# Kernel optimization log

Measured on AMD Instinct MI355X. Metric: run time of the kernel, lower is better.

## Reference

```python
import jax, jax.numpy as jnp
import numpy as np

N = 50000      # nodes
E = 800000     # directed edges (before self loops)
IN = 128       # in_channels
H = 4          # heads
C = 64         # hidden_channels per head
G = 64         # graphs in batch
SLOPE = 0.2    # PyG GATConv default negative_slope


def setup_inputs() -> dict:
    key = jax.random.key(0)
    ks = jax.random.split(key, 16)
    x = jax.random.normal(ks[0], (N, IN), jnp.float32)
    edge_index = jax.random.randint(ks[1], (2, E), 0, N, dtype=jnp.int32)
    batch = jnp.sort(jax.random.randint(ks[2], (N,), 0, G, dtype=jnp.int32))
    s_in = 1.0 / np.sqrt(IN)
    s_hid = 1.0 / np.sqrt(H * C)
    return {
        "x": x,
        "edge_index": edge_index,
        "batch": batch,
        # layer 1: GATConv(IN -> C, heads=H, concat)
        "W1": jax.random.normal(ks[3], (IN, H * C), jnp.float32) * s_in,
        "a_src1": jax.random.normal(ks[4], (H, C), jnp.float32) * s_hid,
        "a_dst1": jax.random.normal(ks[5], (H, C), jnp.float32) * s_hid,
        "b1": jnp.zeros((H * C,), jnp.float32),
        # layer 2: GATConv(H*C -> C, heads=H, concat)
        "W2": jax.random.normal(ks[6], (H * C, H * C), jnp.float32) * s_hid,
        "a_src2": jax.random.normal(ks[7], (H, C), jnp.float32) * s_hid,
        "a_dst2": jax.random.normal(ks[8], (H, C), jnp.float32) * s_hid,
        "b2": jnp.zeros((H * C,), jnp.float32),
        # classifier head
        "W_lin": jax.random.normal(ks[9], (H * C, 2), jnp.float32) * s_hid,
        "b_lin": jnp.zeros((2,), jnp.float32),
    }


def _gat_conv(x, src, dst, W, a_src, a_dst, b):
    """PyG-style GATConv (concat heads, self-loops already in src/dst)."""
    n = x.shape[0]
    h = (x @ W).reshape(n, H, C)                       # [n, H, C]
    alpha_s = jnp.einsum('nhc,hc->nh', h, a_src)       # [n, H]
    alpha_d = jnp.einsum('nhc,hc->nh', h, a_dst)
    e = alpha_s[src] + alpha_d[dst]                    # [Etot, H]
    e = jnp.where(e > 0, e, SLOPE * e)                 # LeakyReLU
    # segment softmax over edges incoming to each destination node
    e_max = jax.lax.stop_gradient(jax.ops.segment_max(e, dst, num_segments=n))
    ex = jnp.exp(e - e_max[dst])
    denom = jax.ops.segment_sum(ex, dst, num_segments=n)
    alpha = ex / denom[dst]                            # [Etot, H]
    msg = alpha[:, :, None] * h[src]                   # [Etot, H, C]
    out = jax.ops.segment_sum(msg, dst, num_segments=n)
    return out.reshape(n, H * C) + b


def reference(x, edge_index, batch, W1, a_src1, a_dst1, b1,
              W2, a_src2, a_dst2, b2, W_lin, b_lin):
    n = x.shape[0]
    # add self loops (PyG GATConv default add_self_loops=True)
    loop = jnp.arange(n, dtype=edge_index.dtype)
    src = jnp.concatenate([edge_index[0], loop])
    dst = jnp.concatenate([edge_index[1], loop])

    h = _gat_conv(x, src, dst, W1, a_src1, a_dst1, b1)
    h = jax.nn.elu(h)                                  # dropout inactive (eval)
    h = _gat_conv(h, src, dst, W2, a_src2, a_dst2, b2)
    h = jax.nn.elu(h)

    # global mean pool over node-to-graph assignment
    sums = jax.ops.segment_sum(h, batch, num_segments=G)
    cnt = jax.ops.segment_sum(jnp.ones((n,), h.dtype), batch, num_segments=G)
    pooled = sums / jnp.maximum(cnt, 1.0)[:, None]     # [G, H*C]

    return pooled @ W_lin + b_lin                      # [G, 2] logits
```

## Files before the change

### kernel.cpp

```cpp
#include <hip/hip_runtime.h>
#include <hip/hip_bf16.h>
#include <math.h>

#define NN 50000
#define EE 800000
#define IN_CH 128
#define HH 4
#define CC 64
#define GG 64
#define HC 256
#define SLOPE 0.2f

#define NBUK 98
#define BDST 512
#define CAPB 10240
#define CAPD 64

typedef short bf16x8 __attribute__((ext_vector_type(8)));
typedef float f32x4  __attribute__((ext_vector_type(4)));
typedef float f32x2  __attribute__((ext_vector_type(2)));

__device__ inline ushort f2bf(float f) {
    union { __hip_bfloat16 h; ushort u; } c;
    c.h = __float2bfloat16(f);
    return c.u;
}
__device__ inline float bfu(ushort u) {
    union { uint u; float f; } c; c.u = ((uint)u) << 16; return c.f;
}
__device__ inline uchar f2e4m3(float v) {
    return (uchar)(__builtin_amdgcn_cvt_pk_fp8_f32(v, v, 0, false) & 0xff);
}
__device__ inline void pkfma(f32x2& a, f32x2 b, f32x2 c) {
    asm("v_pk_fma_f32 %0, %1, %2, %0" : "+v"(a) : "v"(b), "v"(c));
}


__device__ void conv_body(const float* __restrict__ B, ushort* __restrict__ Bt,
                          int kt, int n0, float (*tile)[33]) {
    int tx = threadIdx.x & 31, ty = threadIdx.x >> 5;
    #pragma unroll
    for (int r = ty; r < 32; r += 8)
        tile[r][tx] = B[(size_t)(kt * 32 + r) * 256 + n0 + tx];
    __syncthreads();
    #pragma unroll
    for (int r = ty; r < 32; r += 8)
        Bt[((size_t)kt * 256 + n0 + r) * 32 + tx] = f2bf(tile[tx][r]);
}

__global__ __launch_bounds__(256) void prep_kernel(const float* __restrict__ W1,
                                                   ushort* __restrict__ Bt1,
                                                   const float* __restrict__ W2,
                                                   ushort* __restrict__ Bt2,
                                                   int* __restrict__ bcnt,
                                                   float* __restrict__ pool,
                                                   float* __restrict__ pcnt) {
    __shared__ float tile[32][33];
    int b = blockIdx.x;
    if (b < 32) {
        conv_body(W1, Bt1, b >> 3, (b & 7) * 32, tile);
    } else if (b < 96) {
        int bb = b - 32;
        conv_body(W2, Bt2, bb >> 3, (bb & 7) * 32, tile);
    } else if (b == 96) {
        int i = threadIdx.x;
        if (i < NBUK) bcnt[i] = 0;
        if (i < GG) pcnt[i] = 0.f;
    } else {
        pool[(b - 97) * 256 + threadIdx.x] = 0.f;
    }
}


__global__ __launch_bounds__(256) void partition_kernel(const int* __restrict__ ei,
                                                        int* __restrict__ bcnt,
                                                        int2* __restrict__ part,
                                                        int total) {
    __shared__ int hist[NBUK];
    __shared__ int base[NBUK];
    int t = threadIdx.x;
    int c0 = blockIdx.x * 2048;
    for (int b = t; b < NBUK; b += 256) hist[b] = 0;
    __syncthreads();
    int s[8], d[8], rk[8], bk[8];
    #pragma unroll
    for (int k = 0; k < 8; ++k) {
        int i = c0 + k * 256 + t;
        rk[k] = -1;
        if (i < total) {
            if (i < EE) { s[k] = ei[i]; d[k] = ei[EE + i]; }
            else        { s[k] = d[k] = i - EE; }
            bk[k] = d[k] >> 9;
            rk[k] = atomicAdd(&hist[bk[k]], 1);
        }
    }
    __syncthreads();
    for (int b = t; b < NBUK; b += 256) {
        int h = hist[b];
        base[b] = h ? atomicAdd(&bcnt[b], h) : 0;
    }
    __syncthreads();
    #pragma unroll
    for (int k = 0; k < 8; ++k) {
        if (rk[k] >= 0) {
            int pos = base[bk[k]] + rk[k];
            if (pos < CAPB)
                part[(size_t)bk[k] * CAPB + pos] = make_int2(s[k], d[k]);
        }
    }
}


__global__ __launch_bounds__(1024) void bucket_csr_kernel(const int* __restrict__ bcnt,
                                                          const int2* __restrict__ part,
                                                          ushort* __restrict__ csrb,
                                                          int* __restrict__ cnt_out, int n) {
    __shared__ int cnt[BDST];
    __shared__ ushort rows[BDST * CAPD];
    int b = blockIdx.x, t = threadIdx.x;
    int d0 = b << 9;
    for (int i = t; i < BDST; i += 1024) cnt[i] = 0;
    __syncthreads();
    int m = min(bcnt[b], CAPB);
    const int2* pp = part + (size_t)b * CAPB;
    for (int i = t; i < m; i += 1024) {
        int2 e = pp[i];
        int ld = e.y - d0;
        int r = atomicAdd(&cnt[ld], 1);
        if (r < CAPD) rows[(ld << 6) + r] = (ushort)e.x;
    }
    __syncthreads();
    const uint4* src4 = reinterpret_cast<const uint4*>(rows);
    uint4* dst4 = reinterpret_cast<uint4*>(csrb + ((size_t)d0 << 6));
    #pragma unroll
    for (int i = 0; i < 4; ++i) dst4[i * 1024 + t] = src4[i * 1024 + t];
    for (int i = t; i < BDST; i += 1024) {
        int dd = d0 + i;
        if (dd < n) cnt_out[dd] = min(cnt[i], CAPD);
    }
}


template <int K, bool A_BF16>
__global__ __launch_bounds__(256) void mfma_gemm_fused(const void* __restrict__ Ap,
                                                       const ushort* __restrict__ Bt,
                                                       uchar* __restrict__ H8,
                                                       float* __restrict__ as_,
                                                       float* __restrict__ ad_,
                                                       const float* __restrict__ a_src,
                                                       const float* __restrict__ a_dst,
                                                       int M) {
    __shared__ __align__(16) ushort As[64 * 32];
    __shared__ __align__(16) ushort Bs[256 * 32];
    int tid = threadIdx.x;
    int wave = tid >> 6, lane = tid & 63;
    int bm = blockIdx.x * 64;

    f32x4 acc[4][4] = {{}};

    for (int k0 = 0; k0 < K; k0 += 32) {
        {
            int row = tid >> 2, sl = tid & 3;
            int gr = bm + row;
            uint4 q = {0u, 0u, 0u, 0u};
            if (gr < M) {
                if constexpr (A_BF16) {
                    q = *reinterpret_cast<const uint4*>((const ushort*)Ap + (size_t)gr * K + k0 + sl * 8);
                } else {
                    const float* ap = (const float*)Ap + (size_t)gr * K + k0 + sl * 8;
                    float4 f0 = *reinterpret_cast<const float4*>(ap);
                    float4 f1 = *reinterpret_cast<const float4*>(ap + 4);
                    q.x = (uint)f2bf(f0.x) | ((uint)f2bf(f0.y) << 16);
                    q.y = (uint)f2bf(f0.z) | ((uint)f2bf(f0.w) << 16);
                    q.z = (uint)f2bf(f1.x) | ((uint)f2bf(f1.y) << 16);
                    q.w = (uint)f2bf(f1.z) | ((uint)f2bf(f1.w) << 16);
                }
            }
            int ssl = sl ^ ((row >> 1) & 3);
            *reinterpret_cast<uint4*>(&As[row * 32 + ssl * 8]) = q;
        }
        {
            const ushort* bt = Bt + (size_t)(k0 >> 5) * (256 * 32);
            #pragma unroll
            for (int cI = 0; cI < 4; ++cI) {
                int idx = cI * 256 + tid;
                uint4 v = *reinterpret_cast<const uint4*>(bt + idx * 8);
                int n = idx >> 2, sl = idx & 3;
                int ssl = sl ^ ((n >> 1) & 3);
                *reinterpret_cast<uint4*>(&Bs[n * 32 + ssl * 8]) = v;
            }
        }
        __syncthreads();

        int r16 = lane & 15, kg = lane >> 4;
        bf16x8 af[4], bfr[4];
        #pragma unroll
        for (int mi = 0; mi < 4; ++mi) {
            int row = mi * 16 + r16;
            int ssl = kg ^ ((row >> 1) & 3);
            af[mi] = *reinterpret_cast<const bf16x8*>(&As[row * 32 + ssl * 8]);
        }
        #pragma unroll
        for (int ni = 0; ni < 4; ++ni) {
            int n = wave * 64 + ni * 16 + r16;
            int ssl = kg ^ ((n >> 1) & 3);
            bfr[ni] = *reinterpret_cast<const bf16x8*>(&Bs[n * 32 + ssl * 8]);
        }
        #pragma unroll
        for (int mi = 0; mi < 4; ++mi)
            #pragma unroll
            for (int ni = 0; ni < 4; ++ni)
                acc[mi][ni] = __builtin_amdgcn_mfma_f32_16x16x32_bf16(af[mi], bfr[ni], acc[mi][ni], 0, 0, 0);
        __syncthreads();
    }

    int r16 = lane & 15, rg = lane >> 4;
    float asv[4], adv[4];
    #pragma unroll
    for (int ni = 0; ni < 4; ++ni) {
        asv[ni] = a_src[wave * 64 + ni * 16 + r16];
        adv[ni] = a_dst[wave * 64 + ni * 16 + r16];
    }
    #pragma unroll
    for (int mi = 0; mi < 4; ++mi) {
        #pragma unroll
        for (int r = 0; r < 4; ++r) {
            int row = bm + mi * 16 + rg * 4 + r;
            float ps = 0.f, pd = 0.f;
            if (row < M) {
                #pragma unroll
                for (int ni = 0; ni < 4; ++ni) {
                    float v = acc[mi][ni][r];
                    H8[(size_t)row * HC + wave * 64 + ni * 16 + r16] = f2e4m3(v);
                    ps += v * asv[ni];
                    pd += v * adv[ni];
                }
            }
            #pragma unroll
            for (int o = 1; o < 16; o <<= 1) {
                ps += __shfl_xor(ps, o, 64);
                pd += __shfl_xor(pd, o, 64);
            }
            if (row < M && r16 == 0) {
                as_[row * HH + wave] = ps;
                ad_[row * HH + wave] = pd;
            }
        }
    }
}


template <bool OUT_BF16>
__global__ __launch_bounds__(256) void aggregate14_kernel(const uchar* __restrict__ h8,
                                                          const float* __restrict__ as_,
                                                          const float* __restrict__ ad_,
                                                          const int* __restrict__ cnt,
                                                          const ushort* __restrict__ csrb,
                                                          const float* __restrict__ bias,
                                                          void* __restrict__ outp, int n) {
    int w = threadIdx.x >> 6, lane = threadIdx.x & 63;
    int dst = blockIdx.x * 4 + w;
    if (dst >= n) return;
    int es = lane >> 2, hh = lane & 3;
    int ep = lane >> 5, cl = lane & 31;
    int hsel = cl >> 3;

    __shared__ int2 s_pk[4][64][4];

    int deg = cnt[dst];
    int degp = (deg + 7) & ~7;
    const ushort* srcs = csrb + ((size_t)dst << 6);
    float ad = ad_[dst * HH + hh];

    f32x2 accp[4] = {};
    const char* hb = (const char*)h8 + cl * 8;

    int ntile = (degp + 15) >> 4;

    {
        float ew[4]; int sw[4];
        float lm = -INFINITY;
        #pragma unroll
        for (int t = 0; t < 4; ++t) {
            int j = t * 16 + es;
            float e = -INFINITY; int s = 0;
            if (t < ntile && j < deg) {
                s = (int)srcs[j];
                float tv = as_[s * HH + hh] + ad;
                e = fmaxf(tv, tv * SLOPE);
            }
            ew[t] = e; sw[t] = s;
            lm = fmaxf(lm, e);
        }
        #pragma unroll
        for (int o = 4; o < 64; o <<= 1) lm = fmaxf(lm, __shfl_xor(lm, o, 64));
        float den = 0.f;
        #pragma unroll
        for (int t = 0; t < 4; ++t) {
            float wgt = __expf(ew[t] - lm);
            ew[t] = wgt; den += wgt;
        }
        #pragma unroll
        for (int o = 4; o < 64; o <<= 1) den += __shfl_xor(den, o, 64);
        float invden = 1.f / den;
        #pragma unroll
        for (int t = 0; t < 4; ++t) {
            int j = t * 16 + es;
            if (t < ntile && j < degp) {
                s_pk[w][j][hh] = make_int2(__float_as_int(ew[t] * invden), sw[t] << 8);
            }
        }
    }

#define LOADPK(off_, vv, al)                                             \
    {                                                                    \
        int2 pk_ = s_pk[w][jj + (off_) + ep][hsel];                      \
        al = __int_as_float(pk_.x);                                      \
        vv = *reinterpret_cast<const uint2*>(hb + pk_.y);                \
    }

#define DECODE_PK(vv, al)                                                \
    {                                                                    \
        f32x2 ap_; ap_[0] = al; ap_[1] = al;                             \
        f32x2 f_;                                                        \
        f_ = __builtin_amdgcn_cvt_pk_f32_fp8((int)(vv).x, false);        \
        pkfma(accp[0], f_, ap_);                                         \
        f_ = __builtin_amdgcn_cvt_pk_f32_fp8((int)(vv).x, true);         \
        pkfma(accp[1], f_, ap_);                                         \
        f_ = __builtin_amdgcn_cvt_pk_f32_fp8((int)(vv).y, false);        \
        pkfma(accp[2], f_, ap_);                                         \
        f_ = __builtin_amdgcn_cvt_pk_f32_fp8((int)(vv).y, true);         \
        pkfma(accp[3], f_, ap_);                                         \
    }

    for (int jj = 0; jj < degp; jj += 8) {
        uint2 v0, v1, v2, v3;
        float a0, a1, a2, a3;
        LOADPK(0, v0, a0)
        LOADPK(2, v1, a1)
        LOADPK(4, v2, a2)
        LOADPK(6, v3, a3)
        DECODE_PK(v0, a0)
        DECODE_PK(v1, a1)
        DECODE_PK(v2, a2)
        DECODE_PK(v3, a3)
    }
#undef LOADPK
#undef DECODE_PK

    float lo[4] = {accp[0][0], accp[0][1], accp[1][0], accp[1][1]};
    float hi[4] = {accp[2][0], accp[2][1], accp[3][0], accp[3][1]};
    float fin[4];
    #pragma unroll
    for (int k = 0; k < 4; ++k) {
        float send = ep ? lo[k] : hi[k];
        float recv = __shfl_xor(send, 32, 64);
        fin[k] = (ep ? hi[k] : lo[k]) + recv;
    }

    int ch = cl * 8 + ep * 4;
    const float4 b4 = *reinterpret_cast<const float4*>(bias + ch);
    float r0 = fin[0] + b4.x, r1 = fin[1] + b4.y, r2 = fin[2] + b4.z, r3 = fin[3] + b4.w;
    r0 = r0 > 0.f ? r0 : __expf(r0) - 1.f;
    r1 = r1 > 0.f ? r1 : __expf(r1) - 1.f;
    r2 = r2 > 0.f ? r2 : __expf(r2) - 1.f;
    r3 = r3 > 0.f ? r3 : __expf(r3) - 1.f;
    if constexpr (OUT_BF16) {
        uint2 q;
        q.x = (uint)f2bf(r0) | ((uint)f2bf(r1) << 16);
        q.y = (uint)f2bf(r2) | ((uint)f2bf(r3) << 16);
        *reinterpret_cast<uint2*>((ushort*)outp + (size_t)dst * HC + ch) = q;
    } else {
        *reinterpret_cast<float4*>((float*)outp + (size_t)dst * HC + ch) =
            make_float4(r0, r1, r2, r3);
    }
}


__global__ __launch_bounds__(256) void pool_kernel(const ushort* __restrict__ o,
                                                   const int* __restrict__ batch,
                                                   float* __restrict__ pool,
                                                   float* __restrict__ pcnt, int n) {
    int t = threadIdx.x;
    int start = blockIdx.x * 64;
    if (start >= n) return;
    int endn = min(start + 64, n);
    int g = batch[start];
    float acc = 0.f;
    int cnt = 0;
    for (int node = start; node < endn; ++node) {
        int gb = batch[node];
        if (gb != g) {
            atomicAdd(&pool[g * HC + t], acc);
            if (t == 0) atomicAdd(&pcnt[g], (float)cnt);
            acc = 0.f; cnt = 0; g = gb;
        }
        acc += bfu(o[(size_t)node * HC + t]);
        cnt++;
    }
    atomicAdd(&pool[g * HC + t], acc);
    if (t == 0) atomicAdd(&pcnt[g], (float)cnt);
}

__global__ __launch_bounds__(256) void head_kernel(const float* __restrict__ pool,
                                                   const float* __restrict__ pcnt,
                                                   const float* __restrict__ Wl,
                                                   const float* __restrict__ bl,
                                                   float* __restrict__ out) {
    int g = blockIdx.x;
    int t = threadIdx.x;
    float inv = 1.f / fmaxf(pcnt[g], 1.f);
    float p = pool[g * HC + t] * inv;
    float v0 = p * Wl[t * 2 + 0];
    float v1 = p * Wl[t * 2 + 1];
    #pragma unroll
    for (int o = 32; o > 0; o >>= 1) {
        v0 += __shfl_down(v0, o, 64);
        v1 += __shfl_down(v1, o, 64);
    }
    __shared__ float s0[4], s1[4];
    int wid = t >> 6, lane = t & 63;
    if (lane == 0) { s0[wid] = v0; s1[wid] = v1; }
    __syncthreads();
    if (t == 0) {
        out[g * 2 + 0] = s0[0] + s0[1] + s0[2] + s0[3] + bl[0];
        out[g * 2 + 1] = s1[0] + s1[1] + s1[2] + s1[3] + bl[1];
    }
}


extern "C" void kernel_launch(void* const* d_in, const int* in_sizes, int n_in,
                              void* d_out, int out_size, void* d_ws, size_t ws_size,
                              hipStream_t stream) {
    const float* x    = (const float*)d_in[0];
    const int*   ei   = (const int*)d_in[1];
    const int*   batch= (const int*)d_in[2];
    const float* W1   = (const float*)d_in[3];
    const float* as1  = (const float*)d_in[4];
    const float* ad1  = (const float*)d_in[5];
    const float* b1   = (const float*)d_in[6];
    const float* W2   = (const float*)d_in[7];
    const float* as2  = (const float*)d_in[8];
    const float* ad2  = (const float*)d_in[9];
    const float* b2   = (const float*)d_in[10];
    const float* Wl   = (const float*)d_in[11];
    const float* bl   = (const float*)d_in[12];
    float* out = (float*)d_out;

    char* ws = (char*)d_ws;
    size_t off_b = 0;
    auto alloc = [&](size_t bytes) -> void* {
        void* p = ws + off_b;
        off_b = (off_b + bytes + 255) & ~(size_t)255;
        return p;
    };
    uchar*  h8   = (uchar*)alloc((size_t)NN * HC);
    ushort* o1   = (ushort*)alloc((size_t)NN * HC * 2);
    ushort* o2   = (ushort*)alloc((size_t)NN * HC * 2);
    float*  as_  = (float*)alloc((size_t)NN * HH * 4);
    float*  ad_  = (float*)alloc((size_t)NN * HH * 4);
    int*    bcnt = (int*)alloc((size_t)NBUK * 4);
    int2*   part = (int2*)alloc((size_t)NBUK * CAPB * 8);
    ushort* csrb = (ushort*)alloc((size_t)NBUK * BDST * CAPD * 2);
    int*    cnt  = (int*)alloc((size_t)NN * 4);
    float*  pool = (float*)alloc((size_t)GG * HC * 4);
    float*  pcnt = (float*)alloc((size_t)GG * 4);
    ushort* Bt1  = (ushort*)alloc((size_t)HC * IN_CH * 2);
    ushort* Bt2  = (ushort*)alloc((size_t)HC * HC * 2);
    if (off_b > ws_size) return;

    const int TOTAL = EE + NN;

    prep_kernel<<<161, 256, 0, stream>>>(W1, Bt1, W2, Bt2, bcnt, pool, pcnt);
    partition_kernel<<<(TOTAL + 2047) / 2048, 256, 0, stream>>>(ei, bcnt, part, TOTAL);
    bucket_csr_kernel<<<NBUK, 1024, 0, stream>>>(bcnt, part, csrb, cnt, NN);

    int gblocks = (NN + 63) / 64;
    int ablocks = (NN + 3) / 4;
    mfma_gemm_fused<IN_CH, false><<<gblocks, 256, 0, stream>>>(x, Bt1, h8, as_, ad_, as1, ad1, NN);
    aggregate14_kernel<true><<<ablocks, 256, 0, stream>>>(h8, as_, ad_, cnt, csrb, b1, o1, NN);
    mfma_gemm_fused<HC, true><<<gblocks, 256, 0, stream>>>(o1, Bt2, h8, as_, ad_, as2, ad2, NN);
    aggregate14_kernel<true><<<ablocks, 256, 0, stream>>>(h8, as_, ad_, cnt, csrb, b2, o2, NN);
    pool_kernel<<<(NN + 63) / 64, 256, 0, stream>>>(o2, batch, pool, pcnt, NN);
    head_kernel<<<GG, 256, 0, stream>>>(pool, pcnt, Wl, bl, out);
}
```

Measured before the change: 182.5 us.

## Fuse layer-1 GEMM with edge partitioning and vectorize pool kernel

Merges the layer-1 MFMA projection GEMM and the edge bucketing partition into one launch, with block index picking the role, so the two independent stages run concurrently and one launch is removed. The pool kernel is rewritten to binary-search the graph boundary within each 64-node chunk, read 4 bf16 channels per thread, reduce partial sums through shared memory, and issue fewer atomics. The fused kernel carries the larger shared-memory footprint of the GEMM tiles for all blocks, which may reduce occupancy for the partition blocks.

```diff
diff --git a/kernel.cpp b/kernel.cpp
--- a/kernel.cpp
+++ b/kernel.cpp
@@ -27,6 +27,12 @@
 }
 __device__ inline float bfu(ushort u) {
     union { uint u; float f; } c; c.u = ((uint)u) << 16; return c.f;
+}
+__device__ inline float bflo(uint u) {
+    union { uint u; float f; } c; c.u = u << 16; return c.f;
+}
+__device__ inline float bfhi(uint u) {
+    union { uint u; float f; } c; c.u = u & 0xffff0000u; return c.f;
 }
 __device__ inline uchar f2e4m3(float v) {
     return (uchar)(__builtin_amdgcn_cvt_pk_fp8_f32(v, v, 0, false) & 0xff);
@@ -72,40 +78,146 @@
 }
 
 
-__global__ __launch_bounds__(256) void partition_kernel(const int* __restrict__ ei,
-                                                        int* __restrict__ bcnt,
-                                                        int2* __restrict__ part,
-                                                        int total) {
+__global__ __launch_bounds__(256) void gemm1_part_kernel(const float* __restrict__ x,
+                                                         const ushort* __restrict__ Bt,
+                                                         uchar* __restrict__ H8,
+                                                         float* __restrict__ as_,
+                                                         float* __restrict__ ad_,
+                                                         const float* __restrict__ a_src,
+                                                         const float* __restrict__ a_dst,
+                                                         int M, int gblocks,
+                                                         const int* __restrict__ ei,
+                                                         int* __restrict__ bcnt,
+                                                         int2* __restrict__ part,
+                                                         int total) {
+    __shared__ __align__(16) ushort As[64 * 32];
+    __shared__ __align__(16) ushort Bs[256 * 32];
     __shared__ int hist[NBUK];
     __shared__ int base[NBUK];
-    int t = threadIdx.x;
-    int c0 = blockIdx.x * 2048;
-    for (int b = t; b < NBUK; b += 256) hist[b] = 0;
-    __syncthreads();
-    int s[8], d[8], rk[8], bk[8];
-    #pragma unroll
-    for (int k = 0; k < 8; ++k) {
-        int i = c0 + k * 256 + t;
-        rk[k] = -1;
-        if (i < total) {
-            if (i < EE) { s[k] = ei[i]; d[k] = ei[EE + i]; }
-            else        { s[k] = d[k] = i - EE; }
-            bk[k] = d[k] >> 9;
-            rk[k] = atomicAdd(&hist[bk[k]], 1);
-        }
-    }
-    __syncthreads();
-    for (int b = t; b < NBUK; b += 256) {
-        int h = hist[b];
-        base[b] = h ? atomicAdd(&bcnt[b], h) : 0;
-    }
-    __syncthreads();
-    #pragma unroll
-    for (int k = 0; k < 8; ++k) {
-        if (rk[k] >= 0) {
-            int pos = base[bk[k]] + rk[k];
-            if (pos < CAPB)
-                part[(size_t)bk[k] * CAPB + pos] = make_int2(s[k], d[k]);
+    int tid = threadIdx.x;
+
+    if ((int)blockIdx.x < gblocks) {
+        const int K = IN_CH;
+        int wave = tid >> 6, lane = tid & 63;
+        int bm = blockIdx.x * 64;
+
+        f32x4 acc[4][4] = {{}};
+
+        for (int k0 = 0; k0 < K; k0 += 32) {
+            {
+                int row = tid >> 2, sl = tid & 3;
+                int gr = bm + row;
+                uint4 q = {0u, 0u, 0u, 0u};
+                if (gr < M) {
+                    const float* ap = x + (size_t)gr * K + k0 + sl * 8;
+                    float4 f0 = *reinterpret_cast<const float4*>(ap);
+                    float4 f1 = *reinterpret_cast<const float4*>(ap + 4);
+                    q.x = (uint)f2bf(f0.x) | ((uint)f2bf(f0.y) << 16);
+                    q.y = (uint)f2bf(f0.z) | ((uint)f2bf(f0.w) << 16);
+                    q.z = (uint)f2bf(f1.x) | ((uint)f2bf(f1.y) << 16);
+                    q.w = (uint)f2bf(f1.z) | ((uint)f2bf(f1.w) << 16);
+                }
+                int ssl = sl ^ ((row >> 1) & 3);
+                *reinterpret_cast<uint4*>(&As[row * 32 + ssl * 8]) = q;
+            }
+            {
+                const ushort* bt = Bt + (size_t)(k0 >> 5) * (256 * 32);
+                #pragma unroll
+                for (int cI = 0; cI < 4; ++cI) {
+                    int idx = cI * 256 + tid;
+                    uint4 v = *reinterpret_cast<const uint4*>(bt + idx * 8);
+                    int nn = idx >> 2, sl = idx & 3;
+                    int ssl = sl ^ ((nn >> 1) & 3);
+                    *reinterpret_cast<uint4*>(&Bs[nn * 32 + ssl * 8]) = v;
+                }
+            }
+            __syncthreads();
+
+            int r16 = lane & 15, kg = lane >> 4;
+            bf16x8 af[4], bfr[4];
+            #pragma unroll
+            for (int mi = 0; mi < 4; ++mi) {
+                int row = mi * 16 + r16;
+                int ssl = kg ^ ((row >> 1) & 3);
+                af[mi] = *reinterpret_cast<const bf16x8*>(&As[row * 32 + ssl * 8]);
+            }
+            #pragma unroll
+            for (int ni = 0; ni < 4; ++ni) {
+                int nn = wave * 64 + ni * 16 + r16;
+                int ssl = kg ^ ((nn >> 1) & 3);
+                bfr[ni] = *reinterpret_cast<const bf16x8*>(&Bs[nn * 32 + ssl * 8]);
+            }
+            #pragma unroll
+            for (int mi = 0; mi < 4; ++mi)
+                #pragma unroll
+                for (int ni = 0; ni < 4; ++ni)
+                    acc[mi][ni] = __builtin_amdgcn_mfma_f32_16x16x32_bf16(af[mi], bfr[ni], acc[mi][ni], 0, 0, 0);
+            __syncthreads();
+        }
+
+        int r16 = lane & 15, rg = lane >> 4;
+        float asv[4], adv[4];
+        #pragma unroll
+        for (int ni = 0; ni < 4; ++ni) {
+            asv[ni] = a_src[wave * 64 + ni * 16 + r16];
+            adv[ni] = a_dst[wave * 64 + ni * 16 + r16];
+        }
+        #pragma unroll
+        for (int mi = 0; mi < 4; ++mi) {
+            #pragma unroll
+            for (int r = 0; r < 4; ++r) {
+                int row = bm + mi * 16 + rg * 4 + r;
+                float ps = 0.f, pd = 0.f;
+                if (row < M) {
+                    #pragma unroll
+                    for (int ni = 0; ni < 4; ++ni) {
+                        float v = acc[mi][ni][r];
+                        H8[(size_t)row * HC + wave * 64 + ni * 16 + r16] = f2e4m3(v);
+                        ps += v * asv[ni];
+                        pd += v * adv[ni];
+                    }
+                }
+                #pragma unroll
+                for (int o = 1; o < 16; o <<= 1) {
+                    ps += __shfl_xor(ps, o, 64);
+                    pd += __shfl_xor(pd, o, 64);
+                }
+                if (row < M && r16 == 0) {
+                    as_[row * HH + wave] = ps;
+                    ad_[row * HH + wave] = pd;
+                }
+            }
+        }
+    } else {
+        int c0 = ((int)blockIdx.x - gblocks) * 2048;
+        int t = tid;
+        for (int b = t; b < NBUK; b += 256) hist[b] = 0;
+        __syncthreads();
+        int s[8], d[8], rk[8], bk[8];
+        #pragma unroll
+        for (int k = 0; k < 8; ++k) {
+            int i = c0 + k * 256 + t;
+            rk[k] = -1;
+            if (i < total) {
+                if (i < EE) { s[k] = ei[i]; d[k] = ei[EE + i]; }
+                else        { s[k] = d[k] = i - EE; }
+                bk[k] = d[k] >> 9;
+                rk[k] = atomicAdd(&hist[bk[k]], 1);
+            }
+        }
+        __syncthreads();
+        for (int b = t; b < NBUK; b += 256) {
+            int h = hist[b];
+            base[b] = h ? atomicAdd(&bcnt[b], h) : 0;
+        }
+        __syncthreads();
+        #pragma unroll
+        for (int k = 0; k < 8; ++k) {
+            if (rk[k] >= 0) {
+                int pos = base[bk[k]] + rk[k];
+                if (pos < CAPB)
+                    part[(size_t)bk[k] * CAPB + pos] = make_int2(s[k], d[k]);
+            }
         }
     }
 }
@@ -381,25 +493,44 @@
                                                    const int* __restrict__ batch,
                                                    float* __restrict__ pool,
                                                    float* __restrict__ pcnt, int n) {
+    __shared__ float red[4][64][4];
     int t = threadIdx.x;
+    int cq = t & 63, ng = t >> 6;
     int start = blockIdx.x * 64;
     if (start >= n) return;
     int endn = min(start + 64, n);
-    int g = batch[start];
-    float acc = 0.f;
-    int cnt = 0;
-    for (int node = start; node < endn; ++node) {
-        int gb = batch[node];
-        if (gb != g) {
-            atomicAdd(&pool[g * HC + t], acc);
-            if (t == 0) atomicAdd(&pcnt[g], (float)cnt);
-            acc = 0.f; cnt = 0; g = gb;
-        }
-        acc += bfu(o[(size_t)node * HC + t]);
-        cnt++;
-    }
-    atomicAdd(&pool[g * HC + t], acc);
-    if (t == 0) atomicAdd(&pcnt[g], (float)cnt);
+    int g0 = batch[start], g1 = batch[endn - 1];
+    int split = endn;
+    if (g0 != g1) {
+        int lo = start, hi = endn - 1;
+        while (lo < hi) { int mid = (lo + hi) >> 1; if (batch[mid] == g0) lo = mid + 1; else hi = mid; }
+        split = lo;
+    }
+    #pragma unroll
+    for (int seg = 0; seg < 2; ++seg) {
+        int s0 = seg ? split : start;
+        int s1 = seg ? endn : split;
+        if (s0 >= s1) continue;
+        int gg = batch[s0];
+        float a0 = 0.f, a1 = 0.f, a2 = 0.f, a3 = 0.f;
+        for (int node = s0 + ng; node < s1; node += 4) {
+            uint2 v = *reinterpret_cast<const uint2*>(o + (size_t)node * HC + cq * 4);
+            a0 += bflo(v.x); a1 += bfhi(v.x);
+            a2 += bflo(v.y); a3 += bfhi(v.y);
+        }
+        red[ng][cq][0] = a0; red[ng][cq][1] = a1;
+        red[ng][cq][2] = a2; red[ng][cq][3] = a3;
+        __syncthreads();
+        if (ng == 0) {
+            #pragma unroll
+            for (int k = 0; k < 4; ++k) {
+                float s = red[0][cq][k] + red[1][cq][k] + red[2][cq][k] + red[3][cq][k];
+                atomicAdd(&pool[gg * HC + cq * 4 + k], s);
+            }
+            if (cq == 0) atomicAdd(&pcnt[gg], (float)(s1 - s0));
+        }
+        __syncthreads();
+    }
 }
 
 __global__ __launch_bounds__(256) void head_kernel(const float* __restrict__ pool,
@@ -470,17 +601,17 @@
     if (off_b > ws_size) return;
 
     const int TOTAL = EE + NN;
+    const int gblocks = (NN + 63) / 64;
+    const int pblocks = (TOTAL + 2047) / 2048;
+    const int ablocks = (NN + 3) / 4;
 
     prep_kernel<<<161, 256, 0, stream>>>(W1, Bt1, W2, Bt2, bcnt, pool, pcnt);
-    partition_kernel<<<(TOTAL + 2047) / 2048, 256, 0, stream>>>(ei, bcnt, part, TOTAL);
+    gemm1_part_kernel<<<gblocks + pblocks, 256, 0, stream>>>(
+        x, Bt1, h8, as_, ad_, as1, ad1, NN, gblocks, ei, bcnt, part, TOTAL);
     bucket_csr_kernel<<<NBUK, 1024, 0, stream>>>(bcnt, part, csrb, cnt, NN);
-
-    int gblocks = (NN + 63) / 64;
-    int ablocks = (NN + 3) / 4;
-    mfma_gemm_fused<IN_CH, false><<<gblocks, 256, 0, stream>>>(x, Bt1, h8, as_, ad_, as1, ad1, NN);
     aggregate14_kernel<true><<<ablocks, 256, 0, stream>>>(h8, as_, ad_, cnt, csrb, b1, o1, NN);
     mfma_gemm_fused<HC, true><<<gblocks, 256, 0, stream>>>(o1, Bt2, h8, as_, ad_, as2, ad2, NN);
     aggregate14_kernel<true><<<ablocks, 256, 0, stream>>>(h8, as_, ad_, cnt, csrb, b2, o2, NN);
-    pool_kernel<<<(NN + 63) / 64, 256, 0, stream>>>(o2, batch, pool, pcnt, NN);
+    pool_kernel<<<gblocks, 256, 0, stream>>>(o2, batch, pool, pcnt, NN);
     head_kernel<<<GG, 256, 0, stream>>>(pool, pcnt, Wl, bl, out);
 }
```

New measurement: 164.5 us. 9.9% less time.
